# Kernel optimization log

Hardware: AMD Instinct MI355X
Metric: run time of the kernel (lower is better)

## Reference

```python
import jax, jax.numpy as jnp
import numpy as np

# Forest of complete binary trees in level-order layout: local node ids of
# level l are [2^l - 1, 2^(l+1) - 1); node 0 is the root. Processing levels
# from leaves (l = D-1) to root reproduces dgl.prop_nodes_topo for the
# ChildSum TreeLSTM cell (dropout in eval mode / p=0).

N_TREES, DEPTH, HID, EMB, VOCAB = 8, 15, 128, 128, 32000
T = 2 ** DEPTH - 1  # 32767 nodes per tree


def setup_inputs() -> dict:
    key = jax.random.key(0)
    ks = jax.random.split(key, 6)
    s = 0.1  # keep gates away from hard saturation
    return {
        "wordid": jax.random.randint(ks[0], (N_TREES, T), 0, VOCAB),
        "mask": jnp.ones((N_TREES, T), dtype=jnp.int64) if jax.config.jax_enable_x64 else jnp.ones((N_TREES, T), dtype=jnp.int32),
        "h": jnp.zeros((N_TREES, T, HID), jnp.float32),
        "c": jnp.zeros((N_TREES, T, HID), jnp.float32),
        "emb_table": jax.random.normal(ks[1], (VOCAB, EMB), jnp.float32) * s,
        "W_iou": jax.random.normal(ks[2], (EMB, 3 * HID), jnp.float32) * s,  # (in,out) layout == torch Linear weight.T
        "U_iou": jax.random.normal(ks[3], (HID, 3 * HID), jnp.float32) * s,
        "b_iou": jnp.zeros((3 * HID,), jnp.float32),
        "U_f_w": jax.random.normal(ks[4], (HID, HID), jnp.float32) * s,
        "U_f_b": jnp.zeros((HID,), jnp.float32),
    }


def reference(wordid, mask, h, c, emb_table, W_iou, U_iou, b_iou, U_f_w, U_f_b):
    n_trees, t, hid = h.shape
    depth = int(np.log2(t + 1))
    maskf = mask.astype(h.dtype)[..., None]                      # (B,T,1)
    embeds = emb_table[wordid * mask]                            # (B,T,E)
    iou_base = (embeds @ W_iou) * maskf                          # (B,T,3H)  W_iou(x)*mask
    for l in range(depth - 1, -1, -1):
        ps, pe = 2 ** l - 1, 2 ** (l + 1) - 1                    # this level's nodes
        if l == depth - 1:  # leaves: no reduce; c stays at its initial value
            iou = iou_base[:, ps:pe] + b_iou
            c_in = c[:, ps:pe]
        else:               # internal: gather both children, ChildSum reduce
            cs, ce = 2 ** (l + 1) - 1, 2 ** (l + 2) - 1
            ch = h[:, cs:ce].reshape(n_trees, pe - ps, 2, hid)   # children h
            cc = c[:, cs:ce].reshape(n_trees, pe - ps, 2, hid)   # children c
            h_tild = ch.sum(axis=2)                              # sum over children
            f = jax.nn.sigmoid(ch @ U_f_w + U_f_b)               # per-child forget gate
            c_in = (f * cc).sum(axis=2)
            iou = iou_base[:, ps:pe] + h_tild @ U_iou + b_iou
        i, o, u = jnp.split(iou, 3, axis=-1)
        i, o, u = jax.nn.sigmoid(i), jax.nn.sigmoid(o), jnp.tanh(u)
        c_new = i * u + c_in
        h_new = o * jnp.tanh(c_new)
        h = h.at[:, ps:pe].set(h_new)
        c = c.at[:, ps:pe].set(c_new)
    h_all = h.reshape(n_trees * t, hid)
    return h_all, h_all[0]
```

## Files before the change

kernel.cpp:

```cpp
#include <hip/hip_runtime.h>

#define HID    128
#define NTREES 8
#define DEPTH  15
#define TNODES 32767
#define TM     32

typedef __attribute__((ext_vector_type(8))) short bfrag8;
typedef __attribute__((ext_vector_type(4))) float facc4;
typedef __attribute__((ext_vector_type(4))) unsigned int u32x4;

__device__ __forceinline__ unsigned short f2b(float x) {
  union { float f; unsigned u; } a; a.f = x;
  unsigned r = a.u + 0x7fffu + ((a.u >> 16) & 1u);
  return (unsigned short)(r >> 16);
}
__device__ __forceinline__ float b2f(unsigned short b) {
  union { float f; unsigned u; } a; a.u = ((unsigned)b) << 16;
  return a.f;
}
__device__ __forceinline__ float fast_sigmoid(float x) {
  return __builtin_amdgcn_rcpf(1.0f + __expf(-x));
}
__device__ __forceinline__ float fast_tanh(float x) {
  return 1.0f - 2.0f * __builtin_amdgcn_rcpf(1.0f + __expf(2.0f * x));
}

__device__ __forceinline__ void store8(char* base, int byte, const float* v, float sc) {
  union { unsigned short us[8]; u32x4 q; } p;
  #pragma unroll
  for (int i = 0; i < 8; ++i) p.us[i] = f2b(v[i] * sc);
  *(u32x4*)(base + byte) = p.q;
}

__global__ void prep_weights(const float* __restrict__ W_iou,
                             const float* __restrict__ U_iou,
                             const float* __restrict__ U_f_w,
                             unsigned short* __restrict__ Wt,
                             unsigned short* __restrict__ Ut,
                             unsigned short* __restrict__ Uft) {
  int i = blockIdx.x * 256 + threadIdx.x;
  if (i < 384 * HID) {
    int n = i >> 7, k = i & 127;
    Wt[i] = f2b(W_iou[k * 384 + n]);
    Ut[i] = f2b(U_iou[k * 384 + n]);
  }
  if (i < HID * HID) {
    int n = i >> 7, k = i & 127;
    Uft[i] = f2b(U_f_w[k * HID + n]);
  }
}

template <bool LEAF>
__global__ __launch_bounds__(256, 3)
void tree_level_mfma(const int* __restrict__ wordid,
                     const int* __restrict__ mask,
                     const float* __restrict__ c_init,
                     const float* __restrict__ emb_table,
                     const unsigned short* __restrict__ Wt,
                     const unsigned short* __restrict__ Ut,
                     const unsigned short* __restrict__ Uft,
                     const float* __restrict__ b_iou,
                     const float* __restrict__ U_f_b,
                     float* __restrict__ h_out,
                     const float* __restrict__ c_prev,
                     float* __restrict__ c_cur,
                     int level)
{
  __shared__ __align__(16) char smem[33792];
  __shared__ int gnode_s[TM], chb_s[TM], cpl_s[TM], idx_s[TM];
  __shared__ float mf_s[TM];

  const int tid = threadIdx.x;
  const int R  = NTREES << level;
  const int r0 = blockIdx.x * TM;

  if (tid < TM) {
    int r  = r0 + tid;
    int rr = r < R ? r : R - 1;
    int tree = rr >> level;
    int j    = rr & ((1 << level) - 1);
    int node = (1 << level) - 1 + j;
    int gn   = tree * TNODES + node;
    gnode_s[tid] = gn;
    chb_s[tid]   = gn + node + 1;
    cpl_s[tid]   = (tree << (level + 1)) | (j << 1);
    int mk = mask[gn];
    idx_s[tid] = wordid[gn] * mk;
    mf_s[tid]  = (float)mk;
  }
  __syncthreads();

  for (int s = tid; s < TM * 16; s += 256) {
    int m = s >> 4, sl = s & 15;
    const float* src = emb_table + (size_t)idx_s[m] * HID + sl * 8;
    float v[8];
    *(float4*)(v)     = *(const float4*)(src);
    *(float4*)(v + 4) = *(const float4*)(src + 4);
    int byte = (m * 256 + sl * 16) ^ ((m & 7) << 4);
    store8(smem, byte, v, mf_s[m]);
  }
  if (!LEAF) {
    for (int s = tid; s < 2 * TM * 16; s += 256) {
      int row = s >> 4, sl = s & 15;
      const float* src = h_out + (size_t)(chb_s[row >> 1] + (row & 1)) * HID + sl * 8;
      float v[8];
      *(float4*)(v)     = *(const float4*)(src);
      *(float4*)(v + 4) = *(const float4*)(src + 4);
      int byte = 16384 + ((row * 256 + sl * 16) ^ ((row & 7) << 4));
      store8(smem, byte, v, 1.0f);
    }
    __syncthreads();
    for (int s = tid; s < TM * 16; s += 256) {
      int m = s >> 4, sl = s & 15;
      int b0 = 16384 + (((2 * m) * 256 + sl * 16) ^ (((2 * m) & 7) << 4));
      int b1 = 16384 + (((2 * m + 1) * 256 + sl * 16) ^ (((2 * m + 1) & 7) << 4));
      bfrag8 a = *(const bfrag8*)(smem + b0);
      bfrag8 b = *(const bfrag8*)(smem + b1);
      union { unsigned short us[8]; u32x4 q; } p;
      #pragma unroll
      for (int i = 0; i < 8; ++i)
        p.us[i] = f2b(b2f((unsigned short)a[i]) + b2f((unsigned short)b[i]));
      int byte = 8192 + ((m * 256 + sl * 16) ^ ((m & 7) << 4));
      *(u32x4*)(smem + byte) = p.q;
    }
  }
  __syncthreads();

  const int lane = tid & 63;
  const int w    = tid >> 6;
  const int lrow = lane & 15, lgrp = lane >> 4;

  facc4 acc[2][6];
  #pragma unroll
  for (int rt = 0; rt < 2; ++rt)
    #pragma unroll
    for (int c = 0; c < 6; ++c)
      #pragma unroll
      for (int e = 0; e < 4; ++e) acc[rt][c][e] = 0.f;

  #pragma unroll
  for (int op = 0; op < (LEAF ? 1 : 2); ++op) {
    const char* abase = smem + op * 8192;
    const unsigned short* Bt = op ? Ut : Wt;
    #pragma unroll
    for (int k = 0; k < 4; ++k) {
      bfrag8 af[2];
      #pragma unroll
      for (int rt = 0; rt < 2; ++rt) {
        int row = rt * 16 + lrow;
        af[rt] = *(const bfrag8*)(abase + ((row * 256 + k * 64 + lgrp * 16) ^ ((row & 7) << 4)));
      }
      #pragma unroll
      for (int c = 0; c < 6; ++c) {
        int gct = (c >> 1) * 8 + 2 * w + (c & 1);
        bfrag8 bf = *(const bfrag8*)(Bt + (size_t)(gct * 16 + lrow) * HID + k * 32 + lgrp * 8);
        acc[0][c] = __builtin_amdgcn_mfma_f32_16x16x32_bf16(af[0], bf, acc[0][c], 0, 0, 0);
        acc[1][c] = __builtin_amdgcn_mfma_f32_16x16x32_bf16(af[1], bf, acc[1][c], 0, 0, 0);
      }
    }
  }

  if (!LEAF) {
    facc4 accf[4][2];
    #pragma unroll
    for (int rt = 0; rt < 4; ++rt)
      #pragma unroll
      for (int c = 0; c < 2; ++c)
        #pragma unroll
        for (int e = 0; e < 4; ++e) accf[rt][c][e] = 0.f;
    #pragma unroll
    for (int k = 0; k < 4; ++k) {
      bfrag8 af[4];
      #pragma unroll
      for (int rt = 0; rt < 4; ++rt) {
        int row = rt * 16 + lrow;
        af[rt] = *(const bfrag8*)(smem + 16384 + ((row * 256 + k * 64 + lgrp * 16) ^ ((row & 7) << 4)));
      }
      #pragma unroll
      for (int c = 0; c < 2; ++c) {
        bfrag8 bf = *(const bfrag8*)(Uft + (size_t)((2 * w + c) * 16 + lrow) * HID + k * 32 + lgrp * 8);
        #pragma unroll
        for (int rt = 0; rt < 4; ++rt)
          accf[rt][c] = __builtin_amdgcn_mfma_f32_16x16x32_bf16(af[rt], bf, accf[rt][c], 0, 0, 0);
      }
    }
    __syncthreads();
    float* f_s = (float*)smem;
    #pragma unroll
    for (int c = 0; c < 2; ++c) {
      int d = w * 32 + c * 16 + lrow;
      float fb = U_f_b[d];
      #pragma unroll
      for (int rt = 0; rt < 4; ++rt)
        #pragma unroll
        for (int reg = 0; reg < 4; ++reg) {
          int frow = rt * 16 + 4 * lgrp + reg;
          f_s[frow * 130 + d] = fast_sigmoid(accf[rt][c][reg] + fb);
        }
    }
  }

  const float* f_s = (const float*)smem;
  #pragma unroll
  for (int rt = 0; rt < 2; ++rt) {
    #pragma unroll
    for (int dt = 0; dt < 2; ++dt) {
      int d = w * 32 + dt * 16 + lrow;
      float bi = b_iou[d], bo = b_iou[HID + d], bu = b_iou[2 * HID + d];
      facc4 ci = acc[rt][0 + dt], co = acc[rt][2 + dt], cu = acc[rt][4 + dt];
      #pragma unroll
      for (int reg = 0; reg < 4; ++reg) {
        int m = rt * 16 + 4 * lgrp + reg;
        if (r0 + m >= R) continue;
        float iv = ci[reg] + bi, ov = co[reg] + bo, uv = cu[reg] + bu;
        float cin;
        if (LEAF) {
          cin = c_init[(size_t)gnode_s[m] * HID + d];
        } else {
          int cpl = cpl_s[m];
          cin = f_s[(2 * m) * 130 + d]     * c_prev[(size_t)cpl * HID + d]
              + f_s[(2 * m + 1) * 130 + d] * c_prev[(size_t)(cpl + 1) * HID + d];
        }
        float cn = fmaf(fast_sigmoid(iv), fast_tanh(uv), cin);
        float hn = fast_sigmoid(ov) * fast_tanh(cn);
        c_cur[(size_t)(r0 + m) * HID + d] = cn;
        int gn = gnode_s[m];
        h_out[(size_t)gn * HID + d] = hn;
        if (gn == 0) h_out[(size_t)NTREES * TNODES * HID + d] = hn;
      }
    }
  }
}

extern "C" void kernel_launch(void* const* d_in, const int* in_sizes, int n_in,
                              void* d_out, int out_size, void* d_ws, size_t ws_size,
                              hipStream_t stream) {
  const int*   wordid = (const int*)d_in[0];
  const int*   mask   = (const int*)d_in[1];
  const float* c_init = (const float*)d_in[3];
  const float* emb    = (const float*)d_in[4];
  const float* W_iou  = (const float*)d_in[5];
  const float* U_iou  = (const float*)d_in[6];
  const float* b_iou  = (const float*)d_in[7];
  const float* U_f_w  = (const float*)d_in[8];
  const float* U_f_b  = (const float*)d_in[9];
  float* out = (float*)d_out;

  char* ws = (char*)d_ws;
  unsigned short* Wt  = (unsigned short*)(ws);
  unsigned short* Ut  = (unsigned short*)(ws + 98304);
  unsigned short* Uft = (unsigned short*)(ws + 196608);
  float* bufA = (float*)(ws + 262144);
  float* bufB = (float*)(ws + 262144 + 67108864);

  prep_weights<<<192, 256, 0, stream>>>(W_iou, U_iou, U_f_w, Wt, Ut, Uft);

  for (int l = DEPTH - 1; l >= 0; --l) {
    int R = NTREES << l;
    int blocks = (R + TM - 1) / TM;
    float* ccur  = ((DEPTH - 1 - l) & 1) ? bufB : bufA;
    float* cprev = ((DEPTH - 1 - l) & 1) ? bufA : bufB;
    if (l == DEPTH - 1)
      tree_level_mfma<true><<<blocks, 256, 0, stream>>>(
          wordid, mask, c_init, emb, Wt, Ut, Uft, b_iou, U_f_b, out, nullptr, ccur, l);
    else
      tree_level_mfma<false><<<blocks, 256, 0, stream>>>(
          wordid, mask, c_init, emb, Wt, Ut, Uft, b_iou, U_f_b, out, cprev, ccur, l);
  }
}
```

Baseline: 526.4 us.

## Fuse top tree levels into cooperative kernel and restructure level kernels

Levels 10 down to 0 now run in one cooperative kernel of 256 blocks that uses grid.sync between levels, replacing eleven small launches whose cost is mostly launch and tail latency. The level kernels also move to 512 threads with each wave owning 16 output columns. Embedding fragments now load straight into registers instead of going through LDS, and the child-h sum is done in fp32 before the single bf16 conversion. The forget gates are stored as bf16 in shared memory. This trades launch overhead for grid-wide barriers, which are costly in the top levels where most blocks sit idle, and adds a non-cooperative fallback path.

```diff
diff --git a/kernel.cpp b/kernel.cpp
--- a/kernel.cpp
+++ b/kernel.cpp
@@ -1,10 +1,14 @@
 #include <hip/hip_runtime.h>
+#include <hip/hip_cooperative_groups.h>
+
+namespace cg = cooperative_groups;
 
 #define HID    128
 #define NTREES 8
 #define DEPTH  15
 #define TNODES 32767
 #define TM     32
+#define FUSE_TOP 10
 
 typedef __attribute__((ext_vector_type(8))) short bfrag8;
 typedef __attribute__((ext_vector_type(4))) float facc4;
@@ -25,7 +29,6 @@
 __device__ __forceinline__ float fast_tanh(float x) {
   return 1.0f - 2.0f * __builtin_amdgcn_rcpf(1.0f + __expf(2.0f * x));
 }
-
 __device__ __forceinline__ void store8(char* base, int byte, const float* v, float sc) {
   union { unsigned short us[8]; u32x4 q; } p;
   #pragma unroll
@@ -51,185 +54,292 @@
   }
 }
 
-template <bool LEAF>
-__global__ __launch_bounds__(256, 3)
-void tree_level_mfma(const int* __restrict__ wordid,
-                     const int* __restrict__ mask,
-                     const float* __restrict__ c_init,
-                     const float* __restrict__ emb_table,
-                     const unsigned short* __restrict__ Wt,
-                     const unsigned short* __restrict__ Ut,
-                     const unsigned short* __restrict__ Uft,
-                     const float* __restrict__ b_iou,
-                     const float* __restrict__ U_f_b,
-                     float* __restrict__ h_out,
-                     const float* __restrict__ c_prev,
-                     float* __restrict__ c_cur,
-                     int level)
+__global__ __launch_bounds__(512, 5)
+void leaf_kernel(const int* __restrict__ wordid,
+                 const int* __restrict__ mask,
+                 const float* __restrict__ c_init,
+                 const float* __restrict__ emb_table,
+                 const unsigned short* __restrict__ Wt,
+                 const float* __restrict__ b_iou,
+                 float* __restrict__ h_out,
+                 float* __restrict__ c_cur)
 {
-  __shared__ __align__(16) char smem[33792];
-  __shared__ int gnode_s[TM], chb_s[TM], cpl_s[TM], idx_s[TM];
-  __shared__ float mf_s[TM];
-
   const int tid = threadIdx.x;
-  const int R  = NTREES << level;
+  const int lane = tid & 63, w = tid >> 6;
+  const int lrow = lane & 15, lgrp = lane >> 4;
   const int r0 = blockIdx.x * TM;
-
-  if (tid < TM) {
-    int r  = r0 + tid;
-    int rr = r < R ? r : R - 1;
-    int tree = rr >> level;
-    int j    = rr & ((1 << level) - 1);
-    int node = (1 << level) - 1 + j;
-    int gn   = tree * TNODES + node;
-    gnode_s[tid] = gn;
-    chb_s[tid]   = gn + node + 1;
-    cpl_s[tid]   = (tree << (level + 1)) | (j << 1);
+  const int level = DEPTH - 1;
+  const int nl = 1 << level, ps = nl - 1;
+  const int d = w * 16 + lrow;
+
+  float ci[2][4];
+  #pragma unroll
+  for (int rt = 0; rt < 2; ++rt)
+    #pragma unroll
+    for (int reg = 0; reg < 4; ++reg) {
+      int r = r0 + rt * 16 + 4 * lgrp + reg;
+      size_t gn = (size_t)(r >> level) * TNODES + ps + (r & (nl - 1));
+      ci[rt][reg] = c_init[gn * HID + d];
+    }
+
+  int idxA[2]; float mfA[2];
+  #pragma unroll
+  for (int rt = 0; rt < 2; ++rt) {
+    int r = r0 + rt * 16 + lrow;
+    size_t gn = (size_t)(r >> level) * TNODES + ps + (r & (nl - 1));
     int mk = mask[gn];
-    idx_s[tid] = wordid[gn] * mk;
-    mf_s[tid]  = (float)mk;
-  }
-  __syncthreads();
-
-  for (int s = tid; s < TM * 16; s += 256) {
-    int m = s >> 4, sl = s & 15;
-    const float* src = emb_table + (size_t)idx_s[m] * HID + sl * 8;
+    idxA[rt] = wordid[gn] * mk;
+    mfA[rt] = (float)mk;
+  }
+
+  facc4 acc[2][3];
+  #pragma unroll
+  for (int rt = 0; rt < 2; ++rt)
+    #pragma unroll
+    for (int g = 0; g < 3; ++g)
+      #pragma unroll
+      for (int e = 0; e < 4; ++e) acc[rt][g][e] = 0.f;
+
+  #pragma unroll
+  for (int k = 0; k < 4; ++k) {
+    bfrag8 af[2];
+    #pragma unroll
+    for (int rt = 0; rt < 2; ++rt) {
+      const float* src = emb_table + (size_t)idxA[rt] * HID + k * 32 + lgrp * 8;
+      float v[8];
+      *(float4*)(v)     = *(const float4*)(src);
+      *(float4*)(v + 4) = *(const float4*)(src + 4);
+      union { unsigned short us[8]; bfrag8 b; } p;
+      #pragma unroll
+      for (int i = 0; i < 8; ++i) p.us[i] = f2b(v[i] * mfA[rt]);
+      af[rt] = p.b;
+    }
+    #pragma unroll
+    for (int g = 0; g < 3; ++g) {
+      bfrag8 bf = *(const bfrag8*)(Wt + (size_t)((g * 8 + w) * 16 + lrow) * HID + k * 32 + lgrp * 8);
+      acc[0][g] = __builtin_amdgcn_mfma_f32_16x16x32_bf16(af[0], bf, acc[0][g], 0, 0, 0);
+      acc[1][g] = __builtin_amdgcn_mfma_f32_16x16x32_bf16(af[1], bf, acc[1][g], 0, 0, 0);
+    }
+  }
+
+  const float bi = b_iou[d], bo = b_iou[HID + d], bu = b_iou[2 * HID + d];
+  #pragma unroll
+  for (int rt = 0; rt < 2; ++rt)
+    #pragma unroll
+    for (int reg = 0; reg < 4; ++reg) {
+      int m = rt * 16 + 4 * lgrp + reg;
+      int r = r0 + m;
+      size_t gn = (size_t)(r >> level) * TNODES + ps + (r & (nl - 1));
+      float iv = acc[rt][0][reg] + bi;
+      float ov = acc[rt][1][reg] + bo;
+      float uv = acc[rt][2][reg] + bu;
+      float cn = fmaf(fast_sigmoid(iv), fast_tanh(uv), ci[rt][reg]);
+      float hn = fast_sigmoid(ov) * fast_tanh(cn);
+      c_cur[(size_t)r * HID + d] = cn;
+      h_out[gn * HID + d] = hn;
+    }
+}
+
+__device__ __forceinline__ void nonleaf_body(
+    int level, int r0,
+    const int* __restrict__ wordid, const int* __restrict__ mask,
+    const float* __restrict__ emb_table,
+    const unsigned short* __restrict__ Wt, const unsigned short* __restrict__ Ut,
+    const unsigned short* __restrict__ Uft,
+    const float* __restrict__ b_iou, const float* __restrict__ U_f_b,
+    float* __restrict__ h_out, const float* __restrict__ c_prev,
+    float* __restrict__ c_cur, char* smem)
+{
+  const int tid = threadIdx.x;
+  const int lane = tid & 63, w = tid >> 6;
+  const int lrow = lane & 15, lgrp = lane >> 4;
+  const int nl = 1 << level, ps = nl - 1;
+  const int R = NTREES << level;
+  const int d = w * 16 + lrow;
+
+  for (int s = tid; s < 64 * 16; s += 512) {
+    int row = s >> 4, sl = s & 15;
+    int r = r0 + (row >> 1); if (r >= R) r = R - 1;
+    int tree = r >> level, j = r & (nl - 1);
+    size_t gch = (size_t)tree * TNODES + 2 * (ps + j) + 1 + (row & 1);
+    const float* src = h_out + gch * HID + sl * 8;
     float v[8];
     *(float4*)(v)     = *(const float4*)(src);
     *(float4*)(v + 4) = *(const float4*)(src + 4);
+    int byte = 8192 + ((row * 256 + sl * 16) ^ ((row & 7) << 4));
+    store8(smem, byte, v, 1.0f);
+  }
+  for (int s = tid; s < 32 * 16; s += 512) {
+    int m = s >> 4, sl = s & 15;
+    int r = r0 + m; if (r >= R) r = R - 1;
+    int tree = r >> level, j = r & (nl - 1);
+    size_t gl = (size_t)tree * TNODES + 2 * (ps + j) + 1;
+    const float* s0 = h_out + gl * HID + sl * 8;
+    float v[8], u[8];
+    *(float4*)(v)     = *(const float4*)(s0);
+    *(float4*)(v + 4) = *(const float4*)(s0 + 4);
+    *(float4*)(u)     = *(const float4*)(s0 + HID);
+    *(float4*)(u + 4) = *(const float4*)(s0 + HID + 4);
+    #pragma unroll
+    for (int i = 0; i < 8; ++i) v[i] += u[i];
     int byte = (m * 256 + sl * 16) ^ ((m & 7) << 4);
-    store8(smem, byte, v, mf_s[m]);
-  }
-  if (!LEAF) {
-    for (int s = tid; s < 2 * TM * 16; s += 256) {
-      int row = s >> 4, sl = s & 15;
-      const float* src = h_out + (size_t)(chb_s[row >> 1] + (row & 1)) * HID + sl * 8;
+    store8(smem, byte, v, 1.0f);
+  }
+
+  float cp0[2][4], cp1[2][4];
+  #pragma unroll
+  for (int rt = 0; rt < 2; ++rt)
+    #pragma unroll
+    for (int reg = 0; reg < 4; ++reg) {
+      int r = r0 + rt * 16 + 4 * lgrp + reg; if (r >= R) r = R - 1;
+      int tree = r >> level, j = r & (nl - 1);
+      size_t cpl = ((size_t)tree << (level + 1)) | (size_t)(j << 1);
+      cp0[rt][reg] = c_prev[cpl * HID + d];
+      cp1[rt][reg] = c_prev[(cpl + 1) * HID + d];
+    }
+
+  __syncthreads();
+
+  facc4 accf[4];
+  #pragma unroll
+  for (int rt = 0; rt < 4; ++rt)
+    #pragma unroll
+    for (int e = 0; e < 4; ++e) accf[rt][e] = 0.f;
+  #pragma unroll
+  for (int k = 0; k < 4; ++k) {
+    bfrag8 bf = *(const bfrag8*)(Uft + (size_t)(w * 16 + lrow) * HID + k * 32 + lgrp * 8);
+    #pragma unroll
+    for (int rt = 0; rt < 4; ++rt) {
+      int row = rt * 16 + lrow;
+      bfrag8 af = *(const bfrag8*)(smem + 8192 + ((row * 256 + k * 64 + lgrp * 16) ^ ((row & 7) << 4)));
+      accf[rt] = __builtin_amdgcn_mfma_f32_16x16x32_bf16(af, bf, accf[rt], 0, 0, 0);
+    }
+  }
+  __syncthreads();
+  {
+    unsigned short* fsw = (unsigned short*)(smem + 8192);
+    float fb = U_f_b[d];
+    #pragma unroll
+    for (int rt = 0; rt < 4; ++rt)
+      #pragma unroll
+      for (int reg = 0; reg < 4; ++reg) {
+        int frow = rt * 16 + 4 * lgrp + reg;
+        fsw[frow * HID + d] = f2b(fast_sigmoid(accf[rt][reg] + fb));
+      }
+  }
+
+  int idxA[2]; float mfA[2];
+  #pragma unroll
+  for (int rt = 0; rt < 2; ++rt) {
+    int r = r0 + rt * 16 + lrow; if (r >= R) r = R - 1;
+    size_t gn = (size_t)(r >> level) * TNODES + ps + (r & (nl - 1));
+    int mk = mask[gn];
+    idxA[rt] = wordid[gn] * mk;
+    mfA[rt] = (float)mk;
+  }
+  facc4 acc[2][3];
+  #pragma unroll
+  for (int rt = 0; rt < 2; ++rt)
+    #pragma unroll
+    for (int g = 0; g < 3; ++g)
+      #pragma unroll
+      for (int e = 0; e < 4; ++e) acc[rt][g][e] = 0.f;
+
+  #pragma unroll
+  for (int k = 0; k < 4; ++k) {
+    bfrag8 af[2];
+    #pragma unroll
+    for (int rt = 0; rt < 2; ++rt) {
+      const float* src = emb_table + (size_t)idxA[rt] * HID + k * 32 + lgrp * 8;
       float v[8];
       *(float4*)(v)     = *(const float4*)(src);
       *(float4*)(v + 4) = *(const float4*)(src + 4);
-      int byte = 16384 + ((row * 256 + sl * 16) ^ ((row & 7) << 4));
-      store8(smem, byte, v, 1.0f);
-    }
-    __syncthreads();
-    for (int s = tid; s < TM * 16; s += 256) {
-      int m = s >> 4, sl = s & 15;
-      int b0 = 16384 + (((2 * m) * 256 + sl * 16) ^ (((2 * m) & 7) << 4));
-      int b1 = 16384 + (((2 * m + 1) * 256 + sl * 16) ^ (((2 * m + 1) & 7) << 4));
-      bfrag8 a = *(const bfrag8*)(smem + b0);
-      bfrag8 b = *(const bfrag8*)(smem + b1);
-      union { unsigned short us[8]; u32x4 q; } p;
-      #pragma unroll
-      for (int i = 0; i < 8; ++i)
-        p.us[i] = f2b(b2f((unsigned short)a[i]) + b2f((unsigned short)b[i]));
-      int byte = 8192 + ((m * 256 + sl * 16) ^ ((m & 7) << 4));
-      *(u32x4*)(smem + byte) = p.q;
-    }
-  }
-  __syncthreads();
-
-  const int lane = tid & 63;
-  const int w    = tid >> 6;
-  const int lrow = lane & 15, lgrp = lane >> 4;
-
-  facc4 acc[2][6];
-  #pragma unroll
-  for (int rt = 0; rt < 2; ++rt)
-    #pragma unroll
-    for (int c = 0; c < 6; ++c)
-      #pragma unroll
-      for (int e = 0; e < 4; ++e) acc[rt][c][e] = 0.f;
-
-  #pragma unroll
-  for (int op = 0; op < (LEAF ? 1 : 2); ++op) {
-    const char* abase = smem + op * 8192;
-    const unsigned short* Bt = op ? Ut : Wt;
-    #pragma unroll
-    for (int k = 0; k < 4; ++k) {
-      bfrag8 af[2];
-      #pragma unroll
-      for (int rt = 0; rt < 2; ++rt) {
-        int row = rt * 16 + lrow;
-        af[rt] = *(const bfrag8*)(abase + ((row * 256 + k * 64 + lgrp * 16) ^ ((row & 7) << 4)));
-      }
-      #pragma unroll
-      for (int c = 0; c < 6; ++c) {
-        int gct = (c >> 1) * 8 + 2 * w + (c & 1);
-        bfrag8 bf = *(const bfrag8*)(Bt + (size_t)(gct * 16 + lrow) * HID + k * 32 + lgrp * 8);
-        acc[0][c] = __builtin_amdgcn_mfma_f32_16x16x32_bf16(af[0], bf, acc[0][c], 0, 0, 0);
-        acc[1][c] = __builtin_amdgcn_mfma_f32_16x16x32_bf16(af[1], bf, acc[1][c], 0, 0, 0);
-      }
-    }
-  }
-
-  if (!LEAF) {
-    facc4 accf[4][2];
-    #pragma unroll
-    for (int rt = 0; rt < 4; ++rt)
-      #pragma unroll
-      for (int c = 0; c < 2; ++c)
-        #pragma unroll
-        for (int e = 0; e < 4; ++e) accf[rt][c][e] = 0.f;
-    #pragma unroll
-    for (int k = 0; k < 4; ++k) {
-      bfrag8 af[4];
-      #pragma unroll
-      for (int rt = 0; rt < 4; ++rt) {
-        int row = rt * 16 + lrow;
-        af[rt] = *(const bfrag8*)(smem + 16384 + ((row * 256 + k * 64 + lgrp * 16) ^ ((row & 7) << 4)));
-      }
-      #pragma unroll
-      for (int c = 0; c < 2; ++c) {
-        bfrag8 bf = *(const bfrag8*)(Uft + (size_t)((2 * w + c) * 16 + lrow) * HID + k * 32 + lgrp * 8);
-        #pragma unroll
-        for (int rt = 0; rt < 4; ++rt)
-          accf[rt][c] = __builtin_amdgcn_mfma_f32_16x16x32_bf16(af[rt], bf, accf[rt][c], 0, 0, 0);
-      }
-    }
-    __syncthreads();
-    float* f_s = (float*)smem;
-    #pragma unroll
-    for (int c = 0; c < 2; ++c) {
-      int d = w * 32 + c * 16 + lrow;
-      float fb = U_f_b[d];
-      #pragma unroll
-      for (int rt = 0; rt < 4; ++rt)
-        #pragma unroll
-        for (int reg = 0; reg < 4; ++reg) {
-          int frow = rt * 16 + 4 * lgrp + reg;
-          f_s[frow * 130 + d] = fast_sigmoid(accf[rt][c][reg] + fb);
-        }
-    }
-  }
-
-  const float* f_s = (const float*)smem;
-  #pragma unroll
-  for (int rt = 0; rt < 2; ++rt) {
-    #pragma unroll
-    for (int dt = 0; dt < 2; ++dt) {
-      int d = w * 32 + dt * 16 + lrow;
-      float bi = b_iou[d], bo = b_iou[HID + d], bu = b_iou[2 * HID + d];
-      facc4 ci = acc[rt][0 + dt], co = acc[rt][2 + dt], cu = acc[rt][4 + dt];
-      #pragma unroll
-      for (int reg = 0; reg < 4; ++reg) {
-        int m = rt * 16 + 4 * lgrp + reg;
-        if (r0 + m >= R) continue;
-        float iv = ci[reg] + bi, ov = co[reg] + bo, uv = cu[reg] + bu;
-        float cin;
-        if (LEAF) {
-          cin = c_init[(size_t)gnode_s[m] * HID + d];
-        } else {
-          int cpl = cpl_s[m];
-          cin = f_s[(2 * m) * 130 + d]     * c_prev[(size_t)cpl * HID + d]
-              + f_s[(2 * m + 1) * 130 + d] * c_prev[(size_t)(cpl + 1) * HID + d];
-        }
-        float cn = fmaf(fast_sigmoid(iv), fast_tanh(uv), cin);
-        float hn = fast_sigmoid(ov) * fast_tanh(cn);
-        c_cur[(size_t)(r0 + m) * HID + d] = cn;
-        int gn = gnode_s[m];
-        h_out[(size_t)gn * HID + d] = hn;
-        if (gn == 0) h_out[(size_t)NTREES * TNODES * HID + d] = hn;
-      }
-    }
+      union { unsigned short us[8]; bfrag8 b; } p;
+      #pragma unroll
+      for (int i = 0; i < 8; ++i) p.us[i] = f2b(v[i] * mfA[rt]);
+      af[rt] = p.b;
+    }
+    #pragma unroll
+    for (int g = 0; g < 3; ++g) {
+      bfrag8 bf = *(const bfrag8*)(Wt + (size_t)((g * 8 + w) * 16 + lrow) * HID + k * 32 + lgrp * 8);
+      acc[0][g] = __builtin_amdgcn_mfma_f32_16x16x32_bf16(af[0], bf, acc[0][g], 0, 0, 0);
+      acc[1][g] = __builtin_amdgcn_mfma_f32_16x16x32_bf16(af[1], bf, acc[1][g], 0, 0, 0);
+    }
+  }
+  #pragma unroll
+  for (int k = 0; k < 4; ++k) {
+    bfrag8 af[2];
+    #pragma unroll
+    for (int rt = 0; rt < 2; ++rt) {
+      int row = rt * 16 + lrow;
+      af[rt] = *(const bfrag8*)(smem + ((row * 256 + k * 64 + lgrp * 16) ^ ((row & 7) << 4)));
+    }
+    #pragma unroll
+    for (int g = 0; g < 3; ++g) {
+      bfrag8 bf = *(const bfrag8*)(Ut + (size_t)((g * 8 + w) * 16 + lrow) * HID + k * 32 + lgrp * 8);
+      acc[0][g] = __builtin_amdgcn_mfma_f32_16x16x32_bf16(af[0], bf, acc[0][g], 0, 0, 0);
+      acc[1][g] = __builtin_amdgcn_mfma_f32_16x16x32_bf16(af[1], bf, acc[1][g], 0, 0, 0);
+    }
+  }
+
+  const unsigned short* fsr = (const unsigned short*)(smem + 8192);
+  const float bi = b_iou[d], bo = b_iou[HID + d], bu = b_iou[2 * HID + d];
+  #pragma unroll
+  for (int rt = 0; rt < 2; ++rt)
+    #pragma unroll
+    for (int reg = 0; reg < 4; ++reg) {
+      int m = rt * 16 + 4 * lgrp + reg;
+      int r = r0 + m;
+      if (r >= R) continue;
+      int tree = r >> level, j = r & (nl - 1);
+      size_t gn = (size_t)tree * TNODES + ps + j;
+      float iv = acc[rt][0][reg] + bi;
+      float ov = acc[rt][1][reg] + bo;
+      float uv = acc[rt][2][reg] + bu;
+      float cin = b2f(fsr[(2 * m) * HID + d])     * cp0[rt][reg]
+                + b2f(fsr[(2 * m + 1) * HID + d]) * cp1[rt][reg];
+      float cn = fmaf(fast_sigmoid(iv), fast_tanh(uv), cin);
+      float hn = fast_sigmoid(ov) * fast_tanh(cn);
+      c_cur[(size_t)r * HID + d] = cn;
+      h_out[gn * HID + d] = hn;
+      if (gn == 0) h_out[(size_t)NTREES * TNODES * HID + d] = hn;
+    }
+}
+
+__global__ __launch_bounds__(512, 4)
+void nonleaf_kernel(int level,
+                    const int* __restrict__ wordid, const int* __restrict__ mask,
+                    const float* __restrict__ emb_table,
+                    const unsigned short* __restrict__ Wt, const unsigned short* __restrict__ Ut,
+                    const unsigned short* __restrict__ Uft,
+                    const float* __restrict__ b_iou, const float* __restrict__ U_f_b,
+                    float* __restrict__ h_out, const float* __restrict__ c_prev,
+                    float* __restrict__ c_cur)
+{
+  __shared__ __align__(16) char smem[24576];
+  nonleaf_body(level, blockIdx.x * TM, wordid, mask, emb_table, Wt, Ut, Uft,
+               b_iou, U_f_b, h_out, c_prev, c_cur, smem);
+}
+
+__global__ __launch_bounds__(512, 4)
+void fused_tail_kernel(const int* __restrict__ wordid, const int* __restrict__ mask,
+                       const float* __restrict__ emb_table,
+                       const unsigned short* __restrict__ Wt, const unsigned short* __restrict__ Ut,
+                       const unsigned short* __restrict__ Uft,
+                       const float* __restrict__ b_iou, const float* __restrict__ U_f_b,
+                       float* __restrict__ h_out, float* __restrict__ bufA, float* __restrict__ bufB)
+{
+  __shared__ __align__(16) char smem[24576];
+  cg::grid_group grid = cg::this_grid();
+  for (int l = FUSE_TOP; l >= 0; --l) {
+    int nb = (NTREES << l) / TM; if (nb < 1) nb = 1;
+    if ((int)blockIdx.x < nb) {
+      float* ccur = (l & 1) ? bufB : bufA;
+      const float* cprev = (l & 1) ? bufA : bufB;
+      nonleaf_body(l, blockIdx.x * TM, wordid, mask, emb_table, Wt, Ut, Uft,
+                   b_iou, U_f_b, h_out, cprev, ccur, smem);
+    }
+    grid.sync();
   }
 }
 
@@ -248,24 +358,39 @@
   float* out = (float*)d_out;
 
   char* ws = (char*)d_ws;
-  unsigned short* Wt  = (unsigned short*)(ws);
-  unsigned short* Ut  = (unsigned short*)(ws + 98304);
-  unsigned short* Uft = (unsigned short*)(ws + 196608);
+  const unsigned short* Wt  = (const unsigned short*)(ws);
+  const unsigned short* Ut  = (const unsigned short*)(ws + 98304);
+  const unsigned short* Uft = (const unsigned short*)(ws + 196608);
   float* bufA = (float*)(ws + 262144);
   float* bufB = (float*)(ws + 262144 + 67108864);
 
-  prep_weights<<<192, 256, 0, stream>>>(W_iou, U_iou, U_f_w, Wt, Ut, Uft);
-
-  for (int l = DEPTH - 1; l >= 0; --l) {
-    int R = NTREES << l;
-    int blocks = (R + TM - 1) / TM;
-    float* ccur  = ((DEPTH - 1 - l) & 1) ? bufB : bufA;
-    float* cprev = ((DEPTH - 1 - l) & 1) ? bufA : bufB;
-    if (l == DEPTH - 1)
-      tree_level_mfma<true><<<blocks, 256, 0, stream>>>(
-          wordid, mask, c_init, emb, Wt, Ut, Uft, b_iou, U_f_b, out, nullptr, ccur, l);
-    else
-      tree_level_mfma<false><<<blocks, 256, 0, stream>>>(
-          wordid, mask, c_init, emb, Wt, Ut, Uft, b_iou, U_f_b, out, cprev, ccur, l);
-  }
-}
+  prep_weights<<<192, 256, 0, stream>>>(W_iou, U_iou, U_f_w,
+                                        (unsigned short*)Wt, (unsigned short*)Ut,
+                                        (unsigned short*)Uft);
+
+  leaf_kernel<<<(NTREES << (DEPTH - 1)) / TM, 512, 0, stream>>>(
+      wordid, mask, c_init, emb, Wt, b_iou, out, bufA);
+
+  for (int l = DEPTH - 2; l > FUSE_TOP; --l) {
+    int blocks = (NTREES << l) / TM;
+    float* ccur = (l & 1) ? bufB : bufA;
+    const float* cprev = (l & 1) ? bufA : bufB;
+    nonleaf_kernel<<<blocks, 512, 0, stream>>>(l, wordid, mask, emb, Wt, Ut, Uft,
+                                               b_iou, U_f_b, out, cprev, ccur);
+  }
+
+  void* args[] = {(void*)&wordid, (void*)&mask, (void*)&emb, (void*)&Wt, (void*)&Ut,
+                  (void*)&Uft, (void*)&b_iou, (void*)&U_f_b, (void*)&out,
+                  (void*)&bufA, (void*)&bufB};
+  hipError_t e = hipLaunchCooperativeKernel(reinterpret_cast<void*>(fused_tail_kernel),
+                                            dim3(256), dim3(512), args, 0, stream);
+  if (e != hipSuccess) {
+    for (int l = FUSE_TOP; l >= 0; --l) {
+      int blocks = (NTREES << l) / TM; if (blocks < 1) blocks = 1;
+      float* ccur = (l & 1) ? bufB : bufA;
+      const float* cprev = (l & 1) ? bufA : bufB;
+      nonleaf_kernel<<<blocks, 512, 0, stream>>>(l, wordid, mask, emb, Wt, Ut, Uft,
+                                                 b_iou, U_f_b, out, cprev, ccur);
+    }
+  }
+}
```

After: 862.9 us. 63.9% more time.
